# Kernel optimization log

Hardware: AMD Instinct MI355X
Metric: run time of the kernel (lower is better)

The kernel has to match this reference:

```python
import jax, jax.numpy as jnp
import numpy as np

B, Cin, Cout, H, W = 4, 256, 256, 64, 64
DG, KH, KW = 2, 3, 3        # deformable_groups=2, kernel 3x3
K = KH * KW
CG = Cin // DG


def setup_inputs() -> dict:
    key = jax.random.key(0)
    ks = jax.random.split(key, 4)
    x = jax.random.normal(ks[0], (B, Cin, H, W), jnp.float32)
    # offset/mask-predicting 3x3 conv: 3*DG*K = 54 output channels
    # (small weights so sampled offsets stay in a realistic +-few-pixel range)
    w_off = jax.random.normal(ks[1], (3 * DG * K, Cin, KH, KW), jnp.float32) * 0.01
    b_off = jnp.zeros((3 * DG * K,), jnp.float32)
    weight = jax.random.normal(ks[2], (Cout, Cin, KH, KW), jnp.float32) * (1.0 / np.sqrt(Cin * K))
    bias = jnp.zeros((Cout,), jnp.float32)
    return {"x": x, "w_off": w_off, "b_off": b_off, "weight": weight, "bias": bias}


def _dcn_forward(x, w_off, b_off, weight, bias):
    # 1) predict offsets + modulation mask with a regular 3x3 conv
    om = jax.lax.conv_general_dilated(
        x, w_off, window_strides=(1, 1), padding=((1, 1), (1, 1)),
        dimension_numbers=('NCHW', 'OIHW', 'NCHW'))
    om = om + b_off[None, :, None, None]
    off = om[:, :2 * DG * K].reshape(B, DG, 2, K, H, W)        # [.,.,(dy,dx),k,h,w]
    mask = jax.nn.sigmoid(om[:, 2 * DG * K:]).reshape(B, DG, K, H, W)

    # 2) sampling positions: base grid (stride 1, pad 1, dilation 1) + learned offsets
    ky = jnp.repeat(jnp.arange(KH), KW).astype(jnp.float32)    # [K]
    kx = jnp.tile(jnp.arange(KW), KH).astype(jnp.float32)
    gy = jnp.arange(H, dtype=jnp.float32)
    gx = jnp.arange(W, dtype=jnp.float32)
    py = off[:, :, 0] + (gy[None, None, None, :, None] + ky[None, None, :, None, None] - 1.0)  # [B,DG,K,H,W]
    px = off[:, :, 1] + (gx[None, None, None, None, :] + kx[None, None, :, None, None] - 1.0)

    y0 = jnp.floor(py); x0 = jnp.floor(px)
    wy1 = py - y0; wx1 = px - x0
    wy0 = 1.0 - wy1; wx0 = 1.0 - wx1
    y0i = y0.astype(jnp.int32); x0i = x0.astype(jnp.int32)

    imgf = x.reshape(B, DG, CG, H * W)  # channel groups share their group's offsets

    def gather(iy, ix):
        # zero padding outside the image, as in the DCNv2 CUDA kernel
        valid = ((iy >= 0) & (iy < H) & (ix >= 0) & (ix < W)).astype(x.dtype)  # [B,DG,K,H,W]
        idx = jnp.clip(iy, 0, H - 1) * W + jnp.clip(ix, 0, W - 1)
        idx = idx.reshape(B, DG, K * H * W)
        v = jax.vmap(jax.vmap(lambda im, ii: im[:, ii]))(imgf, idx)  # [B,DG,CG,K*H*W]
        return v.reshape(B, DG, CG, K, H, W) * valid[:, :, None]

    # 3) bilinear interpolation of the 4 corners
    sampled = (gather(y0i,     x0i)     * (wy0 * wx0)[:, :, None]
             + gather(y0i,     x0i + 1) * (wy0 * wx1)[:, :, None]
             + gather(y0i + 1, x0i)     * (wy1 * wx0)[:, :, None]
             + gather(y0i + 1, x0i + 1) * (wy1 * wx1)[:, :, None])
    sampled = sampled * mask[:, :, None]  # modulation (DCNv2)

    # 4) weighted accumulation == grouped contraction over (channel, tap)
    wr = weight.reshape(Cout, DG, CG, K)
    out = jnp.einsum('odck,bdckhw->bohw', wr, sampled) + bias[None, :, None, None]
    return out


def reference(x, w_off, b_off, weight, bias):
    return _dcn_forward(x, w_off, b_off, weight, bias)
```

## Files before the change

### kernel.cpp

```cpp
#include <hip/hip_runtime.h>
#include <cstdint>

#define HW 4096

typedef __attribute__((ext_vector_type(8))) short bf16x8;
typedef __attribute__((ext_vector_type(4))) float f32x4;

__device__ __forceinline__ short f2bf(float f) {
    union { float f; uint32_t u; } v; v.f = f;
    uint32_t u = v.u;
    uint32_t r = (u + 0x7FFFu + ((u >> 16) & 1u)) >> 16;
    return (short)(r & 0xFFFFu);
}
__device__ __forceinline__ uint32_t cvtpk(float lo, float hi) {
    uint32_t r;
    asm("v_cvt_pk_bf16_f32 %0, %1, %2" : "=v"(r) : "v"(lo), "v"(hi));
    return r;
}
__device__ __forceinline__ float blo(uint32_t u) { return __uint_as_float(u << 16); }
__device__ __forceinline__ float bhi(uint32_t u) { return __uint_as_float(u & 0xFFFF0000u); }
__device__ __forceinline__ void glds16(const void* g, void* l) {
    __builtin_amdgcn_global_load_lds(
        (const __attribute__((address_space(1))) void*)g,
        (__attribute__((address_space(3))) void*)l, 16, 0, 0);
}

__global__ __launch_bounds__(256) void k_pre(
    const float* __restrict__ x, const float* __restrict__ weight,
    const float* __restrict__ w_off, unsigned short* __restrict__ xT,
    short* __restrict__ a2r, short* __restrict__ wTb)
{
    const int bid = blockIdx.x;
    if (bid < 1024) {
        __shared__ unsigned short s[64][65];
        const int t = threadIdx.x, lane = t & 63, grp = t >> 6;
        const int hw0 = (bid & 63) * 64, c0 = ((bid >> 6) & 3) * 64, b = bid >> 8;
#pragma unroll
        for (int j = 0; j < 16; ++j) {
            int cc = grp * 16 + j;
            float v = x[((size_t)(b * 256 + c0 + cc)) * HW + hw0 + lane];
            s[cc][lane] = (unsigned short)f2bf(v);
        }
        __syncthreads();
#pragma unroll
        for (int j = 0; j < 16; ++j) {
            int hw2 = grp * 16 + j;
            xT[((size_t)b * HW + hw0 + hw2) * 256 + c0 + lane] = s[lane][hw2];
        }
    } else {
        int e = (bid - 1024) * 256 + threadIdx.x;
        if (e < 589824) {
            int el = e & 7;
            int lane = (e >> 3) & 63;
            int rg = (e >> 9) & 15;
            int ss = (e >> 13) & 3;
            int j = e >> 15;
            int o = rg * 16 + (lane & 15);
            int cch = ss * 32 + (lane >> 4) * 8 + el;
            int dg = j / 9, tap = j - dg * 9;
            a2r[e] = f2bf(weight[o * 2304 + (dg * 128 + cch) * 9 + tap]);
        } else {
            int e2 = e - 589824;
            int o = e2 / 2304, r = e2 - o * 2304;
            int tap = r >> 8, c = r & 255;
            wTb[e2] = (o < 54) ? f2bf(w_off[(o * 256 + c) * 9 + tap]) : (short)0;
        }
    }
}

__global__ __launch_bounds__(256, 4) void k_omgemm(
    const short* __restrict__ wTb, const unsigned short* __restrict__ xT,
    float* __restrict__ om2p)
{
    __shared__ short As[2][64 * 32];
    __shared__ short Bs[2][64 * 32];
    const int t = threadIdx.x;
    const int wid = __builtin_amdgcn_readfirstlane(t >> 6);
    const int lane = t & 63, quad = lane >> 4, l16 = lane & 15;
    const int n0 = blockIdx.x * 64, b = n0 >> 12;
    const int ks = blockIdx.y;
    const int nr = t >> 2;
    const int ksh = (t & 3) * 8;
    const int px = (n0 + nr) & 4095, h = px >> 6, w = px & 63;
    const unsigned short* xb = xT + (size_t)b * HW * 256;
    const int cbase = ks * 18;

    auto loadB = [&](int c) -> uint4 {
        int tap = c >> 3, c0 = (c & 7) * 32;
        int hh = h + tap / 3 - 1, ww = w + tap % 3 - 1;
        uint4 bv = {0u, 0u, 0u, 0u};
        if (hh >= 0 && hh < 64 && ww >= 0 && ww < 64)
            bv = *(const uint4*)(xb + (size_t)(hh * 64 + ww) * 256 + c0 + ksh);
        return bv;
    };

    f32x4 acc[4];
#pragma unroll
    for (int i = 0; i < 4; ++i) acc[i] = (f32x4){0.f, 0.f, 0.f, 0.f};

    uint4 bv[2];
    bv[0] = loadB(cbase);
    glds16(wTb + (size_t)nr * 2304 + cbase * 32 + ksh, &As[0][t * 8]);
    *(uint4*)&Bs[0][t * 8] = bv[0];
    bv[1] = loadB(cbase + 1);

#pragma unroll 2
    for (int i = 0; i < 18; ++i) {
        const int p = i & 1;
        __syncthreads();
        if (i < 17) {
            glds16(wTb + (size_t)nr * 2304 + (cbase + i + 1) * 32 + ksh,
                   &As[1 - p][t * 8]);
            *(uint4*)&Bs[1 - p][t * 8] = bv[(i + 1) & 1];
        }
        if (i + 2 < 18) bv[i & 1] = loadB(cbase + i + 2);
        bf16x8 bf = *(const bf16x8*)&Bs[p][(wid * 16 + l16) * 32 + quad * 8];
#pragma unroll
        for (int mi = 0; mi < 4; ++mi) {
            bf16x8 af = *(const bf16x8*)&As[p][(mi * 16 + l16) * 32 + quad * 8];
            acc[mi] = __builtin_amdgcn_mfma_f32_16x16x32_bf16(af, bf, acc[mi], 0, 0, 0);
        }
    }
    const int n = n0 + wid * 16 + l16;
#pragma unroll
    for (int mi = 0; mi < 4; ++mi)
#pragma unroll
        for (int i = 0; i < 4; ++i)
            om2p[(size_t)(ks * 64 + mi * 16 + quad * 4 + i) * 16384 + n] = acc[mi][i];
}

__global__ __launch_bounds__(512, 4) void k_fused(
    const short* __restrict__ A2r, const unsigned short* __restrict__ xT,
    const float* __restrict__ om2p, const float* __restrict__ b_off,
    const float* __restrict__ bias, float* __restrict__ out)
{
    __shared__ short Bs[2][4][32 * 32];
    __shared__ float4 PlnW[18][32];
    __shared__ int4   PlnI[18][32];
    const int t = threadIdx.x;
    const int wid = __builtin_amdgcn_readfirstlane(t >> 6);
    const int lane = t & 63;
    const int quad = lane >> 4, l16 = lane & 15;
    const int wr = wid;

    const int lin = blockIdx.x;
    const int bn = ((lin & 7) << 6) | (lin >> 3);

    const int n0 = bn * 32, b = n0 >> 12;
    const char* xbb = (const char*)xT + (size_t)b * HW * 512;
    const int px = t >> 4;
    const int cc = (t >> 2) & 3;
    const int q8 = (t & 3) * 8;

    for (int s = wid; s < 18; s += 8) {
        if (lane < 32) {
            const int nn = n0 + lane;
            const int dg = s >= 9 ? 1 : 0, tap = s - dg * 9;
            const int hh = (nn >> 6) & 63, ww2 = nn & 63;
            const int cdy = dg * 18 + tap, cdx = cdy + 9, cms = 36 + dg * 9 + tap;
            float dy = b_off[cdy], dx = b_off[cdx], ms = b_off[cms];
#pragma unroll
            for (int cs2 = 0; cs2 < 4; ++cs2) {
                const float* pp = om2p + (size_t)cs2 * 64 * 16384;
                dy += pp[(size_t)cdy * 16384 + nn];
                dx += pp[(size_t)cdx * 16384 + nn];
                ms += pp[(size_t)cms * 16384 + nn];
            }
            ms = 1.f / (1.f + __expf(-ms));
            float py = dy + (float)(hh + tap / 3 - 1);
            float qx = dx + (float)(ww2 + tap % 3 - 1);
            float y0f = floorf(py), x0f = floorf(qx);
            float wy1 = py - y0f, wx1 = qx - x0f;
            float wy0 = 1.f - wy1, wx0 = 1.f - wx1;
            int y0 = (int)y0f, x0 = (int)x0f;
            int y1 = y0 + 1, x1 = x0 + 1;
            bool vy0 = (y0 >= 0) & (y0 < 64), vy1 = (y1 >= 0) & (y1 < 64);
            bool vx0 = (x0 >= 0) & (x0 < 64), vx1 = (x1 >= 0) & (x1 < 64);
            int cy0 = min(max(y0, 0), 63), cy1 = min(max(y1, 0), 63);
            int cx0 = min(max(x0, 0), 63), cx1 = min(max(x1, 0), 63);
            float4 wv;
            wv.x = (vy0 && vx0) ? wy0 * wx0 * ms : 0.f;
            wv.y = (vy0 && vx1) ? wy0 * wx1 * ms : 0.f;
            wv.z = (vy1 && vx0) ? wy1 * wx0 * ms : 0.f;
            wv.w = (vy1 && vx1) ? wy1 * wx1 * ms : 0.f;
            int4 iv = make_int4((cy0 * 64 + cx0) << 9, (cy0 * 64 + cx1) << 9,
                                (cy1 * 64 + cx0) << 9, (cy1 * 64 + cx1) << 9);
            PlnW[s][lane] = wv;
            PlnI[s][lane] = iv;
        }
    }
    __syncthreads();

    const short* Aw = A2r + (size_t)(wr * 2) * 512 + lane * 8;

    f32x4 acc[2][2];
#pragma unroll
    for (int i = 0; i < 2; ++i)
#pragma unroll
        for (int j = 0; j < 2; ++j) acc[i][j] = (f32x4){0.f, 0.f, 0.f, 0.f};

    float4 pw[2];
    int4 pi[2];
    uint4 g[4];
    uint4 ar[8];

    auto pwload = [&](int S) { pw[S & 1] = PlnW[S][px]; };
    auto piload = [&](int S) { pi[S & 1] = PlnI[S][px]; };
    auto gather = [&](int j) {
        const int cb = ((j >= 9 ? 128 : 0) + cc * 32 + q8) * 2;
        const int4 i4 = pi[j & 1];
        g[0] = *(const uint4*)(xbb + i4.x + cb);
        g[1] = *(const uint4*)(xbb + i4.y + cb);
        g[2] = *(const uint4*)(xbb + i4.z + cb);
        g[3] = *(const uint4*)(xbb + i4.w + cb);
    };
    auto aload = [&](int j) {
#pragma unroll
        for (int ss = 0; ss < 4; ++ss)
#pragma unroll
            for (int mi = 0; mi < 2; ++mi)
                ar[ss * 2 + mi] =
                    *(const uint4*)(Aw + (size_t)(j * 4 + ss) * 8192 + mi * 512);
    };
    const int bsw = ((t & 3) ^ ((px >> 1) & 3)) * 8;
    auto packwrite = [&](int j, int buf) {
        const float4 w4 = pw[j & 1];
        float a0 = w4.x * blo(g[0].x) + w4.y * blo(g[1].x) + w4.z * blo(g[2].x) + w4.w * blo(g[3].x);
        float a1 = w4.x * bhi(g[0].x) + w4.y * bhi(g[1].x) + w4.z * bhi(g[2].x) + w4.w * bhi(g[3].x);
        float a2v = w4.x * blo(g[0].y) + w4.y * blo(g[1].y) + w4.z * blo(g[2].y) + w4.w * blo(g[3].y);
        float a3 = w4.x * bhi(g[0].y) + w4.y * bhi(g[1].y) + w4.z * bhi(g[2].y) + w4.w * bhi(g[3].y);
        float a4 = w4.x * blo(g[0].z) + w4.y * blo(g[1].z) + w4.z * blo(g[2].z) + w4.w * blo(g[3].z);
        float a5 = w4.x * bhi(g[0].z) + w4.y * bhi(g[1].z) + w4.z * bhi(g[2].z) + w4.w * bhi(g[3].z);
        float a6 = w4.x * blo(g[0].w) + w4.y * blo(g[1].w) + w4.z * blo(g[2].w) + w4.w * blo(g[3].w);
        float a7 = w4.x * bhi(g[0].w) + w4.y * bhi(g[1].w) + w4.z * bhi(g[2].w) + w4.w * bhi(g[3].w);
        uint4 o;
        o.x = cvtpk(a0, a1); o.y = cvtpk(a2v, a3);
        o.z = cvtpk(a4, a5); o.w = cvtpk(a6, a7);
        *(uint4*)&Bs[buf][cc][px * 32 + bsw] = o;
    };
    auto mfmaPhase = [&](int p) {
#pragma unroll
        for (int ss = 0; ss < 4; ++ss) {
            bf16x8 bfr[2];
#pragma unroll
            for (int ni = 0; ni < 2; ++ni) {
                const int row = ni * 16 + l16;
                bfr[ni] = *(const bf16x8*)&Bs[p][ss][row * 32 + (quad ^ ((row >> 1) & 3)) * 8];
            }
#pragma unroll
            for (int mi = 0; mi < 2; ++mi) {
                bf16x8 af = *(const bf16x8*)&ar[ss * 2 + mi];
#pragma unroll
                for (int ni = 0; ni < 2; ++ni)
                    acc[mi][ni] = __builtin_amdgcn_mfma_f32_16x16x32_bf16(
                        af, bfr[ni], acc[mi][ni], 0, 0, 0);
            }
        }
    };

    pwload(0);
    piload(0);
    gather(0);
    aload(0);
    packwrite(0, 0);
    pwload(1);
    piload(1);

#pragma unroll 2
    for (int i = 0; i < 18; ++i) {
        const int p = i & 1;
        __syncthreads();
        if (i + 1 < 18) gather(i + 1);
        if (i + 2 < 18) { pwload(i + 2); piload(i + 2); }
        __builtin_amdgcn_sched_barrier(0);
        mfmaPhase(p);
        if (i + 1 < 18) aload(i + 1);
        if (i + 1 < 18) packwrite(i + 1, 1 - p);
    }

    const int m0 = wr * 32;
#pragma unroll
    for (int mi = 0; mi < 2; ++mi)
#pragma unroll
        for (int ni = 0; ni < 2; ++ni) {
            int nn = n0 + ni * 16 + l16;
            int bidx = nn >> 12, hw = nn & 4095;
            float* op = out + (size_t)bidx * 256 * 4096 + hw;
#pragma unroll
            for (int r = 0; r < 4; ++r) {
                int m = m0 + mi * 16 + quad * 4 + r;
                op[(size_t)m * 4096] = acc[mi][ni][r] + bias[m];
            }
        }
}

extern "C" void kernel_launch(void* const* d_in, const int* in_sizes, int n_in,
                              void* d_out, int out_size, void* d_ws, size_t ws_size,
                              hipStream_t stream)
{
    const float* x      = (const float*)d_in[0];
    const float* w_off  = (const float*)d_in[1];
    const float* b_off  = (const float*)d_in[2];
    const float* weight = (const float*)d_in[3];
    const float* bias   = (const float*)d_in[4];
    float* out = (float*)d_out;
    char* ws = (char*)d_ws;

    unsigned short* xT   = (unsigned short*)(ws);
    short*          a2r  = (short*)(ws + 8388608);
    short*          wTb  = (short*)(ws + 9568256);
    float*          om2p = (float*)(ws + 9863168);

    hipLaunchKernelGGL(k_pre, dim3(3904), dim3(256), 0, stream,
                       x, weight, w_off, xT, a2r, wTb);
    hipLaunchKernelGGL(k_omgemm, dim3(256, 4), dim3(256), 0, stream, wTb, xT, om2p);
    hipLaunchKernelGGL(k_fused, dim3(512), dim3(512), 0, stream,
                       a2r, xT, om2p, b_off, bias, out);
}
```

Before: 129.2 us.

## Fuse offset/mask conv GEMM into main deformable-conv kernel prologue

Removes the separate k_omgemm launch and its split-K fp32 partial buffer. Each k_fused block now computes the 54-channel offset/mask 3x3 conv for its own 32 pixels with MFMA, keeping A fragments in registers in a pre-swizzled layout and staging B in swizzled LDS. The result goes to shared memory for the sampling-plan stage. This saves a kernel launch and the global round trip of the partial sums. In exchange every block does a serial full-K (2304) prologue, which adds latency before the main GEMM and raises LDS use.

```diff
diff --git a/kernel.cpp b/kernel.cpp
--- a/kernel.cpp
+++ b/kernel.cpp
@@ -19,16 +19,11 @@
 }
 __device__ __forceinline__ float blo(uint32_t u) { return __uint_as_float(u << 16); }
 __device__ __forceinline__ float bhi(uint32_t u) { return __uint_as_float(u & 0xFFFF0000u); }
-__device__ __forceinline__ void glds16(const void* g, void* l) {
-    __builtin_amdgcn_global_load_lds(
-        (const __attribute__((address_space(1))) void*)g,
-        (__attribute__((address_space(3))) void*)l, 16, 0, 0);
-}
 
 __global__ __launch_bounds__(256) void k_pre(
     const float* __restrict__ x, const float* __restrict__ weight,
     const float* __restrict__ w_off, unsigned short* __restrict__ xT,
-    short* __restrict__ a2r, short* __restrict__ wTb)
+    short* __restrict__ a2r, short* __restrict__ wTb2)
 {
     const int bid = blockIdx.x;
     if (bid < 1024) {
@@ -61,80 +56,25 @@
             a2r[e] = f2bf(weight[o * 2304 + (dg * 128 + cch) * 9 + tap]);
         } else {
             int e2 = e - 589824;
-            int o = e2 / 2304, r = e2 - o * 2304;
-            int tap = r >> 8, c = r & 255;
-            wTb[e2] = (o < 54) ? f2bf(w_off[(o * 256 + c) * 9 + tap]) : (short)0;
-        }
-    }
-}
-
-__global__ __launch_bounds__(256, 4) void k_omgemm(
-    const short* __restrict__ wTb, const unsigned short* __restrict__ xT,
-    float* __restrict__ om2p)
-{
-    __shared__ short As[2][64 * 32];
-    __shared__ short Bs[2][64 * 32];
-    const int t = threadIdx.x;
-    const int wid = __builtin_amdgcn_readfirstlane(t >> 6);
-    const int lane = t & 63, quad = lane >> 4, l16 = lane & 15;
-    const int n0 = blockIdx.x * 64, b = n0 >> 12;
-    const int ks = blockIdx.y;
-    const int nr = t >> 2;
-    const int ksh = (t & 3) * 8;
-    const int px = (n0 + nr) & 4095, h = px >> 6, w = px & 63;
-    const unsigned short* xb = xT + (size_t)b * HW * 256;
-    const int cbase = ks * 18;
-
-    auto loadB = [&](int c) -> uint4 {
-        int tap = c >> 3, c0 = (c & 7) * 32;
-        int hh = h + tap / 3 - 1, ww = w + tap % 3 - 1;
-        uint4 bv = {0u, 0u, 0u, 0u};
-        if (hh >= 0 && hh < 64 && ww >= 0 && ww < 64)
-            bv = *(const uint4*)(xb + (size_t)(hh * 64 + ww) * 256 + c0 + ksh);
-        return bv;
-    };
-
-    f32x4 acc[4];
-#pragma unroll
-    for (int i = 0; i < 4; ++i) acc[i] = (f32x4){0.f, 0.f, 0.f, 0.f};
-
-    uint4 bv[2];
-    bv[0] = loadB(cbase);
-    glds16(wTb + (size_t)nr * 2304 + cbase * 32 + ksh, &As[0][t * 8]);
-    *(uint4*)&Bs[0][t * 8] = bv[0];
-    bv[1] = loadB(cbase + 1);
-
-#pragma unroll 2
-    for (int i = 0; i < 18; ++i) {
-        const int p = i & 1;
-        __syncthreads();
-        if (i < 17) {
-            glds16(wTb + (size_t)nr * 2304 + (cbase + i + 1) * 32 + ksh,
-                   &As[1 - p][t * 8]);
-            *(uint4*)&Bs[1 - p][t * 8] = bv[(i + 1) & 1];
-        }
-        if (i + 2 < 18) bv[i & 1] = loadB(cbase + i + 2);
-        bf16x8 bf = *(const bf16x8*)&Bs[p][(wid * 16 + l16) * 32 + quad * 8];
-#pragma unroll
-        for (int mi = 0; mi < 4; ++mi) {
-            bf16x8 af = *(const bf16x8*)&As[p][(mi * 16 + l16) * 32 + quad * 8];
-            acc[mi] = __builtin_amdgcn_mfma_f32_16x16x32_bf16(af, bf, acc[mi], 0, 0, 0);
-        }
-    }
-    const int n = n0 + wid * 16 + l16;
-#pragma unroll
-    for (int mi = 0; mi < 4; ++mi)
-#pragma unroll
-        for (int i = 0; i < 4; ++i)
-            om2p[(size_t)(ks * 64 + mi * 16 + quad * 4 + i) * 16384 + n] = acc[mi][i];
+            int el = e2 & 7;
+            int lane = (e2 >> 3) & 63;
+            int mi2 = (e2 >> 9) & 3;
+            int c = e2 >> 11;
+            int o = mi2 * 16 + (lane & 15);
+            int k = c * 32 + ((lane >> 4) << 3) + el;
+            int tap = k >> 8, ch = k & 255;
+            wTb2[e2] = (o < 54) ? f2bf(w_off[(o * 256 + ch) * 9 + tap]) : (short)0;
+        }
+    }
 }
 
 __global__ __launch_bounds__(512, 4) void k_fused(
-    const short* __restrict__ A2r, const unsigned short* __restrict__ xT,
-    const float* __restrict__ om2p, const float* __restrict__ b_off,
+    const short* __restrict__ A2r, const short* __restrict__ wTb2,
+    const unsigned short* __restrict__ xT, const float* __restrict__ b_off,
     const float* __restrict__ bias, float* __restrict__ out)
 {
     __shared__ short Bs[2][4][32 * 32];
+    __shared__ float omS[64][32];
     __shared__ float4 PlnW[18][32];
     __shared__ int4   PlnI[18][32];
     const int t = threadIdx.x;
@@ -147,10 +87,71 @@
     const int bn = ((lin & 7) << 6) | (lin >> 3);
 
     const int n0 = bn * 32, b = n0 >> 12;
-    const char* xbb = (const char*)xT + (size_t)b * HW * 512;
+    const unsigned short* xb16 = xT + (size_t)b * HW * 256;
+    const char* xbb = (const char*)xb16;
     const int px = t >> 4;
     const int cc = (t >> 2) & 3;
     const int q8 = (t & 3) * 8;
+
+    const int qo  = t >> 7;
+    const int px2 = (t >> 2) & 31;
+    const int ksh2 = (t & 3) * 8;
+    const int nn2 = n0 + px2;
+    const int ph = (nn2 & 4095) >> 6, pw_ = nn2 & 63;
+    const int bsw2 = ((t & 3) ^ ((px2 >> 1) & 3)) * 8;
+    const int mi2 = wid & 3, ni2 = wid >> 2;
+    const short* AwOm = wTb2 + mi2 * 512 + lane * 8;
+
+    f32x4 accOm = (f32x4){0.f, 0.f, 0.f, 0.f};
+    uint4 arOm[4];
+    uint4 gv;
+
+    auto omload = [&](int gi) -> uint4 {
+        const int c = gi * 4 + qo;
+        const int tap = c >> 3, c0 = (c & 7) * 32;
+        const int hh = ph + tap / 3 - 1, ww = pw_ + tap % 3 - 1;
+        uint4 bv = {0u, 0u, 0u, 0u};
+        if (hh >= 0 && hh < 64 && ww >= 0 && ww < 64)
+            bv = *(const uint4*)(xb16 + (size_t)(hh * 64 + ww) * 256 + c0 + ksh2);
+        return bv;
+    };
+    auto aloadOm = [&](int gi) {
+#pragma unroll
+        for (int q = 0; q < 4; ++q)
+            arOm[q] = *(const uint4*)(AwOm + (size_t)(gi * 4 + q) * 2048);
+    };
+
+    gv = omload(0);
+    *(uint4*)&Bs[0][qo][px2 * 32 + bsw2] = gv;
+    aloadOm(0);
+
+#pragma unroll 2
+    for (int gi = 0; gi < 18; ++gi) {
+        const int p = gi & 1;
+        __syncthreads();
+        if (gi + 1 < 18) gv = omload(gi + 1);
+        __builtin_amdgcn_sched_barrier(0);
+#pragma unroll
+        for (int q = 0; q < 4; ++q) {
+            const int row = ni2 * 16 + l16;
+            bf16x8 bq = *(const bf16x8*)&Bs[p][q][row * 32 + (quad ^ ((row >> 1) & 3)) * 8];
+            accOm = __builtin_amdgcn_mfma_f32_16x16x32_bf16(
+                *(const bf16x8*)&arOm[q], bq, accOm, 0, 0, 0);
+        }
+        if (gi + 1 < 18) {
+            *(uint4*)&Bs[1 - p][qo][px2 * 32 + bsw2] = gv;
+            aloadOm(gi + 1);
+        }
+    }
+    __syncthreads();
+    {
+        const int mrow = mi2 * 16 + (lane >> 4) * 4;
+        const int pcol = ni2 * 16 + l16;
+#pragma unroll
+        for (int rr = 0; rr < 4; ++rr)
+            omS[mrow + rr][pcol] = accOm[rr];
+    }
+    __syncthreads();
 
     for (int s = wid; s < 18; s += 8) {
         if (lane < 32) {
@@ -158,14 +159,9 @@
             const int dg = s >= 9 ? 1 : 0, tap = s - dg * 9;
             const int hh = (nn >> 6) & 63, ww2 = nn & 63;
             const int cdy = dg * 18 + tap, cdx = cdy + 9, cms = 36 + dg * 9 + tap;
-            float dy = b_off[cdy], dx = b_off[cdx], ms = b_off[cms];
-#pragma unroll
-            for (int cs2 = 0; cs2 < 4; ++cs2) {
-                const float* pp = om2p + (size_t)cs2 * 64 * 16384;
-                dy += pp[(size_t)cdy * 16384 + nn];
-                dx += pp[(size_t)cdx * 16384 + nn];
-                ms += pp[(size_t)cms * 16384 + nn];
-            }
+            float dy = b_off[cdy] + omS[cdy][lane];
+            float dx = b_off[cdx] + omS[cdx][lane];
+            float ms = b_off[cms] + omS[cms][lane];
             ms = 1.f / (1.f + __expf(-ms));
             float py = dy + (float)(hh + tap / 3 - 1);
             float qx = dx + (float)(ww2 + tap % 3 - 1);
@@ -308,12 +304,10 @@
 
     unsigned short* xT   = (unsigned short*)(ws);
     short*          a2r  = (short*)(ws + 8388608);
-    short*          wTb  = (short*)(ws + 9568256);
-    float*          om2p = (float*)(ws + 9863168);
+    short*          wTb2 = (short*)(ws + 9568256);
 
     hipLaunchKernelGGL(k_pre, dim3(3904), dim3(256), 0, stream,
-                       x, weight, w_off, xT, a2r, wTb);
-    hipLaunchKernelGGL(k_omgemm, dim3(256, 4), dim3(256), 0, stream, wTb, xT, om2p);
+                       x, weight, w_off, xT, a2r, wTb2);
     hipLaunchKernelGGL(k_fused, dim3(512), dim3(512), 0, stream,
-                       a2r, xT, om2p, b_off, bias, out);
-}
+                       a2r, wTb2, xT, b_off, bias, out);
+}
```

Result: faster. 124.9 us (-3.3%).
